# Performance work log

Measured on AMD Instinct MI355X. Metric: run time of the kernel, lower is better.

## Reference

```python
import jax, jax.numpy as jnp
import numpy as np

STRIDE = 2
PADDING = 1


def setup_inputs() -> dict:
    key = jax.random.key(0)
    k1, k2, k3, k4, k5 = jax.random.split(key, 5)
    B, C, H, W = 32, 128, 64, 64
    O, kh, kw = 256, 3, 3
    ah = H + 2 * PADDING - (kh - 1)  # 64
    oh = ah // STRIDE                # 32 (divisible -> ceil == floor, rest == 0)
    inputs = {
        "input": jax.random.normal(k1, (B, C, H, W), dtype=jnp.float32),
        "weight": jax.random.normal(k2, (O, C, kh, kw), dtype=jnp.float32) * 0.05,
        "bias": jax.random.normal(k3, (O,), dtype=jnp.float32) * 0.05,
        "selh": jax.random.randint(k4, (oh, oh), 0, STRIDE, dtype=jnp.int32),
        "selw": jax.random.randint(k5, (oh, oh), 0, STRIDE, dtype=jnp.int32),
    }
    return inputs


def reference(input, weight, bias, selh, selw):
    # Faithful to SConv2dAvg.forward with stoch=True, mask == -1, stride=2:
    # unfold(input, k, pad, stride=1) -> stochastic gather of one position per
    # stride x stride cell (offsets selh/selw) -> GEMM with flattened weight -> reshape.
    B, C, H, W = input.shape
    O, _, kh, kw = weight.shape
    ah = H + 2 * PADDING - (kh - 1)
    aw = W + 2 * PADDING - (kw - 1)
    oh = ah // STRIDE  # divisible by construction; ceil_mode correction is a no-op
    ow = aw // STRIDE
    xp = jnp.pad(input, ((0, 0), (0, 0), (PADDING, PADDING), (PADDING, PADDING)))
    # selected unfold positions in the afterconv grid
    rng_h = selh + (jnp.arange(oh, dtype=selh.dtype) * STRIDE)[:, None]   # [oh, ow]
    rng_w = selw + (jnp.arange(ow, dtype=selw.dtype) * STRIDE)[None, :]   # [oh, ow]
    # gather k x k patches directly (equivalent to gathering unfold columns)
    rows = rng_h[:, :, None, None] + jnp.arange(kh)[None, None, :, None]  # [oh, ow, kh, 1]
    cols = rng_w[:, :, None, None] + jnp.arange(kw)[None, None, None, :]  # [oh, ow, 1, kw]
    patches = xp[:, :, rows, cols]  # [B, C, oh, ow, kh, kw]
    out = jnp.einsum('bchwij,ocij->bohw', patches, weight) + bias[None, :, None, None]
    return out  # [B, O, oh, ow]
```

## Files before the change

### kernel.cpp

```cpp
#include <hip/hip_runtime.h>
#include <hip/hip_bf16.h>


typedef short bf16x8 __attribute__((ext_vector_type(8)));
typedef float f32x4  __attribute__((ext_vector_type(4)));

#define KSTEPS 18
#define WPRE_BYTES (KSTEPS * 256 * 64 * 2)
#define TRANS_BYTES (32 * 66 * 66 * 128 * 2)
#define TOTAL_WS (WPRE_BYTES + TRANS_BYTES)

__device__ __forceinline__ unsigned short f2bf(float x) {
  unsigned u = __float_as_uint(x);
  return (unsigned short)((u + 0x7fffu + ((u >> 16) & 1u)) >> 16);
}
__device__ __forceinline__ unsigned pk2(float a, float b) {
  unsigned ua = __float_as_uint(a), ub = __float_as_uint(b);
  return ((ua + 0x7fffu + ((ua >> 16) & 1u)) >> 16) |
         ((ub + 0x7fffu + ((ub >> 16) & 1u)) & 0xffff0000u);
}
__device__ __forceinline__ bf16x8 ld_frag(const uint4* a) {
  union { uint4 u; bf16x8 s; } cv; cv.u = *a; return cv.s;
}
__device__ __forceinline__ void async16(const void* g, void* l) {
  __builtin_amdgcn_global_load_lds(
      (__attribute__((address_space(1))) void*)(void*)g,
      (__attribute__((address_space(3))) void*)l, 16, 0, 0);
}

__global__ __launch_bounds__(256) void prep(const float* __restrict__ in,
                                            const float* __restrict__ w,
                                            unsigned short* __restrict__ tp,
                                            unsigned short* __restrict__ wpre) {
  const int tid = threadIdx.x;
  if (blockIdx.x >= 66) {
    const int kk = blockIdx.x - 66;
    const int ob = blockIdx.y;
#pragma unroll
    for (int e = 0; e < 2; ++e) {
      int t2   = (tid << 1) + e;
      int o    = (ob << 3) + (t2 >> 6);
      int k_in = t2 & 63;
      int kg   = (kk << 6) + (k_in ^ ((o & 7) << 3));
      int tap  = kg >> 7;
      int c    = kg & 127;
      int di   = (tap >= 6) ? 2 : ((tap >= 3) ? 1 : 0);
      int dj   = tap - di * 3;
      wpre[(kk << 14) + (o << 6) + k_in] = f2bf(w[(o * 128 + c) * 9 + di * 3 + dj]);
    }
    return;
  }
  __shared__ float lds[128 * 65];
  const int hp = blockIdx.x;
  const int b  = blockIdx.y;
  uint4* rowp = (uint4*)(tp + (size_t)(b * 66 + hp) * 66 * 128);
  uint4 z; z.x = z.y = z.z = z.w = 0u;
  if (hp == 0 || hp == 65) {
    for (int s = tid; s < 1056; s += 256) rowp[s] = z;
    return;
  }
  const int h = hp - 1;
  const float* src = in + ((size_t)b << 19) + (h << 6);
  const int ww = tid & 63, c0 = tid >> 6;
#pragma unroll
  for (int pass = 0; pass < 32; ++pass) {
    int c = (pass << 2) + c0;
    lds[c * 65 + ww] = src[((size_t)c << 12) + ww];
  }
  __syncthreads();
  for (int s = tid; s < 1056; s += 256) {
    if (s < 16 || s >= 1040) { rowp[s] = z; continue; }
    int idx = s - 16;
    int wq = idx >> 4, c8 = idx & 15;
    const float* lp = lds + (c8 << 3) * 65 + wq;
    uint4 d;
    d.x = pk2(lp[0],   lp[65]);
    d.y = pk2(lp[130], lp[195]);
    d.z = pk2(lp[260], lp[325]);
    d.w = pk2(lp[390], lp[455]);
    rowp[s] = d;
  }
}

__global__ __launch_bounds__(512, 4) void sconv_mfma3(
    const unsigned short* __restrict__ tp,
    const unsigned short* __restrict__ wpre,
    const float* __restrict__ bias,
    const int* __restrict__ selh,
    const int* __restrict__ selw,
    float* __restrict__ out)
{
  __shared__ uint4 Alds[2][1024];
  __shared__ uint4 Blds[2][1024];
  __shared__ float bias_s[128];

  const int tid = threadIdx.x;
  const int d    = blockIdx.x;
  const int blk  = ((d & 7) << 6) + (d >> 3);
  const int b     = blk >> 4;
  const int y0    = ((blk >> 1) & 7) << 2;
  const int ohalf = blk & 1;

  if (tid < 128) bias_s[tid] = bias[(ohalf << 7) + tid];

  const int p0 = tid >> 3;
  const int sl = tid & 7;
  int addr0, addr1;
  {
    const int py0 = y0 + (p0 >> 5);
    const int px  = p0 & 31;
    const int sh0 = selh[(py0 << 5) | px], sw0 = selw[(py0 << 5) | px];
    const int py1 = py0 + 2;
    const int sh1 = selh[(py1 << 5) | px], sw1 = selw[(py1 << 5) | px];
    addr0 = (b * 66 + 2 * py0 + sh0) * 66 + 2 * px + sw0;
    addr1 = (b * 66 + 2 * py1 + sh1) * 66 + 2 * px + sw1;
  }
  const int n0 = sl ^ (p0 & 7);
  const char* tbase = (const char*)tp;

  const int wv = tid >> 6, ln = tid & 63;
  const int wo = wv & 1;
  const int wp = wv >> 1;
  const int lo = ln & 15, hi = ln >> 4;

  const char* wsrc = (const char*)wpre + (ohalf << 14) + (tid << 4);

  f32x4 acc[4][2] = {};

#define STAGE(BUF, KK)                                                        \
  do {                                                                        \
    const int tap_ = (KK) >> 1;                                               \
    const int di_  = (tap_ >= 6) ? 2 : ((tap_ >= 3) ? 1 : 0);                 \
    const int dj_  = tap_ - 3 * di_;                                          \
    const int toff_ = ((di_ * 66 + dj_) << 8) + (((KK) & 1) << 7) + (n0 << 4);\
    uint4* A_ = &Alds[BUF][0];                                                \
    uint4* B_ = &Blds[BUF][0];                                                \
    async16(tbase + ((size_t)addr0 << 8) + toff_, A_ + (wv << 6));            \
    async16(tbase + ((size_t)addr1 << 8) + toff_, A_ + (wv << 6) + 512);      \
    async16(wsrc + ((KK) << 15),        B_ + (wv << 6));                      \
    async16(wsrc + ((KK) << 15) + 8192, B_ + (wv << 6) + 512);                \
  } while (0)

  STAGE(0, 0);
  int cur = 0;

  for (int kk = 0; kk < KSTEPS; ++kk) {
    if (kk < KSTEPS - 1) {
      STAGE(cur ^ 1, kk + 1);
      asm volatile("s_waitcnt vmcnt(4)" ::: "memory");
    } else {
      asm volatile("s_waitcnt vmcnt(0)" ::: "memory");
    }
    __builtin_amdgcn_s_barrier();
    asm volatile("" ::: "memory");

    const uint4* A = &Alds[cur][0];
    const uint4* B = &Blds[cur][0];
    bf16x8 FW[4][2], FP[2][2];
#pragma unroll
    for (int f = 0; f < 4; ++f) {
      const int orow = (wo << 6) + (f << 4) + lo;
#pragma unroll
      for (int ks = 0; ks < 2; ++ks)
        FW[f][ks] = ld_frag(B + (orow << 3) + (((ks << 2) | hi) ^ (orow & 7)));
    }
#pragma unroll
    for (int f = 0; f < 2; ++f) {
      const int prow = (wp << 5) + (f << 4) + lo;
#pragma unroll
      for (int ks = 0; ks < 2; ++ks)
        FP[f][ks] = ld_frag(A + (prow << 3) + (((ks << 2) | hi) ^ (prow & 7)));
    }
#pragma unroll
    for (int fo = 0; fo < 4; ++fo)
#pragma unroll
      for (int fp = 0; fp < 2; ++fp)
#pragma unroll
        for (int ks = 0; ks < 2; ++ks)
          acc[fo][fp] = __builtin_amdgcn_mfma_f32_16x16x32_bf16(
              FW[fo][ks], FP[fp][ks], acc[fo][fp], 0, 0, 0);

    asm volatile("s_waitcnt lgkmcnt(0)" ::: "memory");
    __builtin_amdgcn_s_barrier();
    asm volatile("" ::: "memory");
    cur ^= 1;
  }
#undef STAGE

  float* ob = out + ((size_t)b << 18) + ((size_t)ohalf << 17) + (y0 << 5);
#pragma unroll
  for (int fo = 0; fo < 4; ++fo) {
    const int obase = (wo << 6) + (fo << 4) + (hi << 2);
#pragma unroll
    for (int fp = 0; fp < 2; ++fp) {
      const int pix = (wp << 5) + (fp << 4) + lo;
#pragma unroll
      for (int j = 0; j < 4; ++j) {
        const int o = obase + j;
        ob[((size_t)o << 10) + pix] = acc[fo][fp][j] + bias_s[o];
      }
    }
  }
}

__global__ __launch_bounds__(256) void sconv_naive(
    const float* __restrict__ in, const float* __restrict__ w,
    const float* __restrict__ bias, const int* __restrict__ selh,
    const int* __restrict__ selw, float* __restrict__ out) {
  int idx = (blockIdx.x << 8) + threadIdx.x;
  if (idx >= 32 * 256 * 32 * 32) return;
  int x = idx & 31, y = (idx >> 5) & 31, o = (idx >> 10) & 255, b = idx >> 18;
  int rh0 = 2 * y + selh[(y << 5) | x] - 1;
  int rw0 = 2 * x + selw[(y << 5) | x] - 1;
  const float* inb = in + ((size_t)b << 19);
  const float* wo_ = w + o * 1152;
  float acc = bias[o];
  for (int c = 0; c < 128; ++c)
    for (int i = 0; i < 3; ++i) {
      int rh = rh0 + i;
      if (rh < 0 || rh >= 64) continue;
      for (int j = 0; j < 3; ++j) {
        int rw = rw0 + j;
        if (rw < 0 || rw >= 64) continue;
        acc += inb[(c << 12) + (rh << 6) + rw] * wo_[c * 9 + i * 3 + j];
      }
    }
  out[idx] = acc;
}

extern "C" void kernel_launch(void* const* d_in, const int* in_sizes, int n_in,
                              void* d_out, int out_size, void* d_ws, size_t ws_size,
                              hipStream_t stream) {
  const float* in   = (const float*)d_in[0];
  const float* w    = (const float*)d_in[1];
  const float* bias = (const float*)d_in[2];
  const int*   selh = (const int*)d_in[3];
  const int*   selw = (const int*)d_in[4];
  float* out = (float*)d_out;

  if (ws_size >= (size_t)TOTAL_WS) {
    unsigned short* wpre = (unsigned short*)d_ws;
    unsigned short* tp   = (unsigned short*)((char*)d_ws + WPRE_BYTES);
    prep<<<dim3(84, 32), dim3(256), 0, stream>>>(in, w, tp, wpre);
    sconv_mfma3<<<dim3(512), dim3(512), 0, stream>>>(tp, wpre, bias, selh, selw, out);
  } else {
    sconv_naive<<<dim3(32768), dim3(256), 0, stream>>>(in, w, bias, selh, selw, out);
  }
}
```

Baseline: 47.74 us.

## Use 4-stage K32 LDS pipeline with one barrier per step, vectorize prep loads

The main GEMM kernel now uses a K-step of 32 instead of 64 and splits LDS into four buffers, so loads run two steps ahead. Each step issues one A and one B async load per thread and has a single barrier instead of two. The weight pre-layout and its XOR swizzle are changed to match the narrower K chunk, and the input transpose reads float4 instead of scalars. Half-size steps mean twice as many barriers and waits per tile, and it is unclear whether deeper prefetch hides latency better than the larger MFMA batches it replaces.

After: 45.31 us. 1.05x faster.

```diff
diff --git a/kernel.cpp b/kernel.cpp
--- a/kernel.cpp
+++ b/kernel.cpp
@@ -5,8 +5,8 @@
 typedef short bf16x8 __attribute__((ext_vector_type(8)));
 typedef float f32x4  __attribute__((ext_vector_type(4)));
 
-#define KSTEPS 18
-#define WPRE_BYTES (KSTEPS * 256 * 64 * 2)
+#define NSTEP 36
+#define WPRE_BYTES (NSTEP * 256 * 32 * 2)
 #define TRANS_BYTES (32 * 66 * 66 * 128 * 2)
 #define TOTAL_WS (WPRE_BYTES + TRANS_BYTES)
 
@@ -34,20 +34,15 @@
                                             unsigned short* __restrict__ wpre) {
   const int tid = threadIdx.x;
   if (blockIdx.x >= 66) {
-    const int kk = blockIdx.x - 66;
-    const int ob = blockIdx.y;
-#pragma unroll
-    for (int e = 0; e < 2; ++e) {
-      int t2   = (tid << 1) + e;
-      int o    = (ob << 3) + (t2 >> 6);
-      int k_in = t2 & 63;
-      int kg   = (kk << 6) + (k_in ^ ((o & 7) << 3));
-      int tap  = kg >> 7;
-      int c    = kg & 127;
-      int di   = (tap >= 6) ? 2 : ((tap >= 3) ? 1 : 0);
-      int dj   = tap - di * 3;
-      wpre[(kk << 14) + (o << 6) + k_in] = f2bf(w[(o * 128 + c) * 9 + di * 3 + dj]);
-    }
+    const int s    = blockIdx.x - 66;
+    const int o    = (blockIdx.y << 3) + (tid >> 5);
+    const int k_in = tid & 31;
+    const int kg   = (s << 5) + (((k_in >> 3) ^ ((o >> 1) & 3)) << 3) + (k_in & 7);
+    const int tap  = kg >> 7;
+    const int c    = kg & 127;
+    const int di   = (tap >= 6) ? 2 : ((tap >= 3) ? 1 : 0);
+    const int dj   = tap - di * 3;
+    wpre[(s << 13) + (o << 5) + k_in] = f2bf(w[(o * 128 + c) * 9 + di * 3 + dj]);
     return;
   }
   __shared__ float lds[128 * 65];
@@ -61,11 +56,14 @@
   }
   const int h = hp - 1;
   const float* src = in + ((size_t)b << 19) + (h << 6);
-  const int ww = tid & 63, c0 = tid >> 6;
-#pragma unroll
-  for (int pass = 0; pass < 32; ++pass) {
-    int c = (pass << 2) + c0;
-    lds[c * 65 + ww] = src[((size_t)c << 12) + ww];
+  const int ww4 = (tid & 15) << 2;
+  const int c0  = tid >> 4;
+#pragma unroll
+  for (int pass = 0; pass < 8; ++pass) {
+    int c = (pass << 4) + c0;
+    float4 v = *(const float4*)(src + ((size_t)c << 12) + ww4);
+    float* lp = lds + c * 65 + ww4;
+    lp[0] = v.x; lp[1] = v.y; lp[2] = v.z; lp[3] = v.w;
   }
   __syncthreads();
   for (int s = tid; s < 1056; s += 256) {
@@ -82,7 +80,7 @@
   }
 }
 
-__global__ __launch_bounds__(512, 4) void sconv_mfma3(
+__global__ __launch_bounds__(512, 4) void sconv_mfma4(
     const unsigned short* __restrict__ tp,
     const unsigned short* __restrict__ wpre,
     const float* __restrict__ bias,
@@ -90,32 +88,29 @@
     const int* __restrict__ selw,
     float* __restrict__ out)
 {
-  __shared__ uint4 Alds[2][1024];
-  __shared__ uint4 Blds[2][1024];
+  __shared__ uint4 Alds[4][512];
+  __shared__ uint4 Blds[4][512];
   __shared__ float bias_s[128];
 
   const int tid = threadIdx.x;
-  const int d    = blockIdx.x;
-  const int blk  = ((d & 7) << 6) + (d >> 3);
+  const int d0    = blockIdx.x;
+  const int blk   = ((d0 & 7) << 6) + (d0 >> 3);
   const int b     = blk >> 4;
   const int y0    = ((blk >> 1) & 7) << 2;
   const int ohalf = blk & 1;
 
   if (tid < 128) bias_s[tid] = bias[(ohalf << 7) + tid];
 
-  const int p0 = tid >> 3;
-  const int sl = tid & 7;
-  int addr0, addr1;
+  const int p0 = tid >> 2;
+  const int sl = tid & 3;
+  int addr0;
   {
-    const int py0 = y0 + (p0 >> 5);
-    const int px  = p0 & 31;
-    const int sh0 = selh[(py0 << 5) | px], sw0 = selw[(py0 << 5) | px];
-    const int py1 = py0 + 2;
-    const int sh1 = selh[(py1 << 5) | px], sw1 = selw[(py1 << 5) | px];
-    addr0 = (b * 66 + 2 * py0 + sh0) * 66 + 2 * px + sw0;
-    addr1 = (b * 66 + 2 * py1 + sh1) * 66 + 2 * px + sw1;
-  }
-  const int n0 = sl ^ (p0 & 7);
+    const int py = y0 + (p0 >> 5);
+    const int px = p0 & 31;
+    addr0 = (b * 66 + 2 * py + selh[(py << 5) | px]) * 66
+          + 2 * px + selw[(py << 5) | px];
+  }
+  const int u0 = sl ^ ((p0 >> 1) & 3);
   const char* tbase = (const char*)tp;
 
   const int wv = tid >> 6, ln = tid & 63;
@@ -123,69 +118,68 @@
   const int wp = wv >> 1;
   const int lo = ln & 15, hi = ln >> 4;
 
-  const char* wsrc = (const char*)wpre + (ohalf << 14) + (tid << 4);
+  const char* wsrc = (const char*)wpre + (ohalf << 13) + (tid << 4);
 
   f32x4 acc[4][2] = {};
 
 #define STAGE(BUF, KK)                                                        \
   do {                                                                        \
-    const int tap_ = (KK) >> 1;                                               \
+    const int tap_ = (KK) >> 2;                                               \
     const int di_  = (tap_ >= 6) ? 2 : ((tap_ >= 3) ? 1 : 0);                 \
     const int dj_  = tap_ - 3 * di_;                                          \
-    const int toff_ = ((di_ * 66 + dj_) << 8) + (((KK) & 1) << 7) + (n0 << 4);\
-    uint4* A_ = &Alds[BUF][0];                                                \
-    uint4* B_ = &Blds[BUF][0];                                                \
-    async16(tbase + ((size_t)addr0 << 8) + toff_, A_ + (wv << 6));            \
-    async16(tbase + ((size_t)addr1 << 8) + toff_, A_ + (wv << 6) + 512);      \
-    async16(wsrc + ((KK) << 15),        B_ + (wv << 6));                      \
-    async16(wsrc + ((KK) << 15) + 8192, B_ + (wv << 6) + 512);                \
+    const int toff_ = ((di_ * 66 + dj_) << 8) + (((KK) & 3) << 6) + (u0 << 4);\
+    async16(tbase + ((size_t)addr0 << 8) + toff_, &Alds[BUF][wv << 6]);       \
+    async16(wsrc + ((KK) << 14), &Blds[BUF][wv << 6]);                        \
   } while (0)
 
+#define DO_MMA(BUF)                                                           \
+  do {                                                                        \
+    const uint4* A_ = &Alds[BUF][0];                                          \
+    const uint4* B_ = &Blds[BUF][0];                                          \
+    bf16x8 FW[4], FP[2];                                                      \
+    _Pragma("unroll")                                                         \
+    for (int f = 0; f < 4; ++f) {                                             \
+      const int orow = (wo << 6) + (f << 4) + lo;                             \
+      FW[f] = ld_frag(B_ + (orow << 2) + (hi ^ ((orow >> 1) & 3)));           \
+    }                                                                         \
+    _Pragma("unroll")                                                         \
+    for (int f = 0; f < 2; ++f) {                                             \
+      const int prow = (wp << 5) + (f << 4) + lo;                             \
+      FP[f] = ld_frag(A_ + (prow << 2) + (hi ^ ((prow >> 1) & 3)));           \
+    }                                                                         \
+    _Pragma("unroll")                                                         \
+    for (int fo = 0; fo < 4; ++fo)                                            \
+      _Pragma("unroll")                                                       \
+      for (int fp = 0; fp < 2; ++fp)                                          \
+        acc[fo][fp] = __builtin_amdgcn_mfma_f32_16x16x32_bf16(                \
+            FW[fo], FP[fp], acc[fo][fp], 0, 0, 0);                            \
+  } while (0)
+
   STAGE(0, 0);
-  int cur = 0;
-
-  for (int kk = 0; kk < KSTEPS; ++kk) {
-    if (kk < KSTEPS - 1) {
-      STAGE(cur ^ 1, kk + 1);
-      asm volatile("s_waitcnt vmcnt(4)" ::: "memory");
-    } else {
-      asm volatile("s_waitcnt vmcnt(0)" ::: "memory");
-    }
+  STAGE(1, 1);
+
+#pragma unroll 4
+  for (int kk = 0; kk < NSTEP - 2; ++kk) {
+    STAGE((kk + 2) & 3, kk + 2);
+    asm volatile("s_waitcnt vmcnt(4)" ::: "memory");
     __builtin_amdgcn_s_barrier();
     asm volatile("" ::: "memory");
-
-    const uint4* A = &Alds[cur][0];
-    const uint4* B = &Blds[cur][0];
-    bf16x8 FW[4][2], FP[2][2];
-#pragma unroll
-    for (int f = 0; f < 4; ++f) {
-      const int orow = (wo << 6) + (f << 4) + lo;
-#pragma unroll
-      for (int ks = 0; ks < 2; ++ks)
-        FW[f][ks] = ld_frag(B + (orow << 3) + (((ks << 2) | hi) ^ (orow & 7)));
-    }
-#pragma unroll
-    for (int f = 0; f < 2; ++f) {
-      const int prow = (wp << 5) + (f << 4) + lo;
-#pragma unroll
-      for (int ks = 0; ks < 2; ++ks)
-        FP[f][ks] = ld_frag(A + (prow << 3) + (((ks << 2) | hi) ^ (prow & 7)));
-    }
-#pragma unroll
-    for (int fo = 0; fo < 4; ++fo)
-#pragma unroll
-      for (int fp = 0; fp < 2; ++fp)
-#pragma unroll
-        for (int ks = 0; ks < 2; ++ks)
-          acc[fo][fp] = __builtin_amdgcn_mfma_f32_16x16x32_bf16(
-              FW[fo][ks], FP[fp][ks], acc[fo][fp], 0, 0, 0);
-
+    DO_MMA(kk & 3);
     asm volatile("s_waitcnt lgkmcnt(0)" ::: "memory");
-    __builtin_amdgcn_s_barrier();
-    asm volatile("" ::: "memory");
-    cur ^= 1;
-  }
+  }
+
+  asm volatile("s_waitcnt vmcnt(2)" ::: "memory");
+  __builtin_amdgcn_s_barrier();
+  asm volatile("" ::: "memory");
+  DO_MMA(2);
+  asm volatile("s_waitcnt lgkmcnt(0)" ::: "memory");
+
+  asm volatile("s_waitcnt vmcnt(0)" ::: "memory");
+  __builtin_amdgcn_s_barrier();
+  asm volatile("" ::: "memory");
+  DO_MMA(3);
 #undef STAGE
+#undef DO_MMA
 
   float* ob = out + ((size_t)b << 18) + ((size_t)ohalf << 17) + (y0 << 5);
 #pragma unroll
@@ -241,8 +235,8 @@
   if (ws_size >= (size_t)TOTAL_WS) {
     unsigned short* wpre = (unsigned short*)d_ws;
     unsigned short* tp   = (unsigned short*)((char*)d_ws + WPRE_BYTES);
-    prep<<<dim3(84, 32), dim3(256), 0, stream>>>(in, w, tp, wpre);
-    sconv_mfma3<<<dim3(512), dim3(512), 0, stream>>>(tp, wpre, bias, selh, selw, out);
+    prep<<<dim3(102, 32), dim3(256), 0, stream>>>(in, w, tp, wpre);
+    sconv_mfma4<<<dim3(512), dim3(512), 0, stream>>>(tp, wpre, bias, selh, selw, out);
   } else {
     sconv_naive<<<dim3(32768), dim3(256), 0, stream>>>(in, w, bias, selh, selw, out);
   }
```
